# Performance work log

Measured on AMD Instinct MI355X. Metric: run time of the kernel, lower is better.

The kernel has to match this reference:

```python
import jax, jax.numpy as jnp
import numpy as np

M = 64            # multiplicity of 0e and 1o node irreps
NODE_DIM = M + 3 * M  # 256
NUM_BASIS = 8
CUTOFF = 5.0
HIDDEN = 64
NUM_W = 4 * M     # tp weight_numel: 4 uvu paths, M weights each
EPS = 1e-5


def setup_inputs() -> dict:
    key = jax.random.key(0)
    ks = jax.random.split(key, 16)
    N, E = 40000, 640000
    node_feats = jax.random.normal(ks[0], (N, NODE_DIM), dtype=jnp.float32)
    edge_index = jax.random.randint(ks[1], (2, E), 0, N)
    edge_vectors = jax.random.normal(ks[2], (E, 3), dtype=jnp.float32)
    edge_lengths = jax.random.uniform(ks[3], (E,), minval=0.5, maxval=CUTOFF, dtype=jnp.float32)
    # radial MLP params (num_basis -> hidden -> hidden -> NUM_W, SiLU)
    mlp_w1 = jax.random.normal(ks[4], (NUM_BASIS, HIDDEN), dtype=jnp.float32) / np.sqrt(NUM_BASIS)
    mlp_b1 = jnp.zeros((HIDDEN,), jnp.float32)
    mlp_w2 = jax.random.normal(ks[5], (HIDDEN, HIDDEN), dtype=jnp.float32) / np.sqrt(HIDDEN)
    mlp_b2 = jnp.zeros((HIDDEN,), jnp.float32)
    mlp_w3 = jax.random.normal(ks[6], (HIDDEN, NUM_W), dtype=jnp.float32) / np.sqrt(HIDDEN)
    mlp_b3 = jnp.zeros((NUM_W,), jnp.float32)
    # equivariant linear: per-irrep channel mixing
    lin_w0 = jax.random.normal(ks[7], (M, M), dtype=jnp.float32)
    lin_w1 = jax.random.normal(ks[8], (M, M), dtype=jnp.float32)
    # equivariant layer norm affine params
    gamma0 = jnp.ones((M,), jnp.float32)
    beta0 = jnp.zeros((M,), jnp.float32)
    gamma1 = jnp.ones((M,), jnp.float32)
    return dict(node_feats=node_feats, edge_index=edge_index, edge_vectors=edge_vectors,
                edge_lengths=edge_lengths, mlp_w1=mlp_w1, mlp_b1=mlp_b1, mlp_w2=mlp_w2,
                mlp_b2=mlp_b2, mlp_w3=mlp_w3, mlp_b3=mlp_b3, lin_w0=lin_w0, lin_w1=lin_w1,
                gamma0=gamma0, beta0=beta0, gamma1=gamma1)


def reference(node_feats, edge_index, edge_vectors, edge_lengths,
              mlp_w1, mlp_b1, mlp_w2, mlp_b2, mlp_w3, mlp_b3,
              lin_w0, lin_w1, gamma0, beta0, gamma1):
    N = node_feats.shape[0]
    row, col = edge_index[0], edge_index[1]

    # spherical harmonics of normalized edge vectors, 'component' normalization
    unit = edge_vectors / jnp.linalg.norm(edge_vectors, axis=-1, keepdims=True)
    sh1 = jnp.sqrt(3.0) * unit                                     # [E,3]; sh0 == 1

    # Bessel radial basis on edge lengths
    n = jnp.arange(1, NUM_BASIS + 1, dtype=node_feats.dtype)
    r = edge_lengths[:, None]
    rbf = jnp.sqrt(2.0 / CUTOFF) * jnp.sin(n * jnp.pi * r / CUTOFF) / r  # [E,B]

    # polynomial envelope (DimeNet, p=5)
    u = edge_lengths / CUTOFF
    env = jnp.where(u < 1.0, 1.0 - 21.0 * u**5 + 35.0 * u**6 - 15.0 * u**7, 0.0)[:, None]

    # radial MLP -> per-edge tensor-product weights, enveloped
    h = jax.nn.silu(rbf @ mlp_w1 + mlp_b1)
    h = jax.nn.silu(h @ mlp_w2 + mlp_b2)
    tp_w = (h @ mlp_w3 + mlp_b3) * env                             # [E, 4M]
    wa, wb, wc, wd = jnp.split(tp_w, 4, axis=-1)                   # each [E,M]

    # gather sender features
    s0 = node_feats[row, :M]                                       # [E,M]   0e block
    s1 = node_feats[row, M:].reshape(-1, M, 3)                     # [E,M,3] 1o block

    # weighted uvu tensor product, path-normalized (2 paths per output irrep)
    inv_s2 = 1.0 / jnp.sqrt(2.0)
    m0 = (wa * s0 + wd * jnp.einsum('emi,ei->em', s1, sh1)) * inv_s2        # [E,M]
    m1 = (wb[:, :, None] * s1 + wc[:, :, None] * s0[:, :, None] * sh1[:, None, :]) * inv_s2
    messages = jnp.concatenate([m0, m1.reshape(-1, 3 * M)], axis=-1)        # [E,256]

    # scatter-add to receivers
    agg = jax.ops.segment_sum(messages, col, num_segments=N)       # [N,256]

    # equivariant linear: mix multiplicities per irrep, fan-in normalized
    a0 = (agg[:, :M] @ lin_w0) / jnp.sqrt(jnp.asarray(M, node_feats.dtype))
    a1 = jnp.einsum('nmi,mk->nki', agg[:, M:].reshape(N, M, 3), lin_w1) \
         / jnp.sqrt(jnp.asarray(M, node_feats.dtype))

    # equivariant layer norm: standard LN on scalars, RMS-of-norms on vectors
    mu = a0.mean(axis=-1, keepdims=True)
    var = ((a0 - mu) ** 2).mean(axis=-1, keepdims=True)
    o0 = gamma0 * (a0 - mu) / jnp.sqrt(var + EPS) + beta0
    vnorm2 = (a1 ** 2).sum(-1)                                     # [N,M]
    rms = jnp.sqrt(vnorm2.mean(-1, keepdims=True) + EPS)           # [N,1]
    o1 = gamma1[None, :, None] * a1 / rms[:, :, None]

    out = jnp.concatenate([o0, o1.reshape(N, 3 * M)], axis=-1)
    return node_feats + out
```

## Files before the change

kernel.cpp:

```cpp
#include <hip/hip_runtime.h>
#include <hip/hip_fp16.h>

#define NDIM 256
#define LUT_N 2048
#define LUT_BLOCKS (LUT_N / 4)
#define SCAN_BLK 1024

typedef _Float16 h2 __attribute__((ext_vector_type(2)));
union HU { unsigned u; h2 h; };

__device__ __forceinline__ float fdot2f(unsigned a_bits, unsigned b_bits, float c)
{
    HU a, b; a.u = a_bits; b.u = b_bits;
#if __has_builtin(__builtin_amdgcn_fdot2)
    return __builtin_amdgcn_fdot2(a.h, b.h, c, false);
#else
    return fmaf((float)a.h.x, (float)b.h.x, fmaf((float)a.h.y, (float)b.h.y, c));
#endif
}

__global__ __launch_bounds__(256) void prep_kernel(
    const float* __restrict__ w1, const float* __restrict__ b1,
    const float* __restrict__ w2, const float* __restrict__ b2,
    const float* __restrict__ w3, const float* __restrict__ b3,
    uint4* __restrict__ lutp,
    const int* __restrict__ col, int E,
    int* __restrict__ counts, int* __restrict__ rank,
    const float* __restrict__ nf, uint2* __restrict__ nft,
    int histBlocks, int N)
{
    if (blockIdx.x >= (unsigned)(LUT_BLOCKS + histBlocks)) {
        int t = (blockIdx.x - LUT_BLOCKS - histBlocks) * 256 + threadIdx.x;
        if (t < N * 64) {
            int n = t >> 6, m = t & 63;
            const float* nr = nf + (size_t)n * NDIM;
            float s0 = nr[m];
            float3 s1 = ((const float3*)(nr + 64))[m];
            HU a, b;
            a.h = h2{(_Float16)s1.x, (_Float16)s1.y};
            b.h = h2{(_Float16)s1.z, (_Float16)s0};
            nft[t] = make_uint2(a.u, b.u);
        }
        return;
    }
    if (blockIdx.x >= (unsigned)LUT_BLOCKS) {
        int i = (blockIdx.x - LUT_BLOCKS) * 256 + threadIdx.x;
        if (i < E) rank[i] = atomicAdd(&counts[col[i]], 1);
        return;
    }

    __shared__ float h1[4][2][64];
    __shared__ float hh2[4][2][64];
    int tid = threadIdx.x;
    int wave = tid >> 6;
    int j = tid & 63;
    int p = blockIdx.x * 4 + wave;
    int pn = (p < LUT_N - 1) ? p + 1 : p;
    const float step = 4.5f / (float)(LUT_N - 1);
    float ra = 0.5f + step * (float)p;
    float rb = 0.5f + step * (float)pn;

    const float cnorm = 0.6324555320336759f;
    float acca = b1[j], accb = acca;
    #pragma unroll
    for (int k = 0; k < 8; ++k) {
        float freq = (float)(k + 1) * (3.14159265358979323846f / 5.0f);
        float wv = w1[k * 64 + j];
        acca = fmaf(cnorm * sinf(freq * ra) / ra, wv, acca);
        accb = fmaf(cnorm * sinf(freq * rb) / rb, wv, accb);
    }
    h1[wave][0][j] = acca / (1.0f + expf(-acca));
    h1[wave][1][j] = accb / (1.0f + expf(-accb));
    __syncthreads();

    acca = b2[j]; accb = acca;
    #pragma unroll 8
    for (int m = 0; m < 64; ++m) {
        float wv = w2[m * 64 + j];
        acca = fmaf(h1[wave][0][m], wv, acca);
        accb = fmaf(h1[wave][1][m], wv, accb);
    }
    hh2[wave][0][j] = acca / (1.0f + expf(-acca));
    hh2[wave][1][j] = accb / (1.0f + expf(-accb));
    __syncthreads();

    float ua = ra * 0.2f, ub = rb * 0.2f;
    float ua5 = ua * ua * ua * ua * ua, ub5 = ub * ub * ub * ub * ub;
    float enva = (ua < 1.0f) ? (1.0f - 21.0f * ua5 + 35.0f * ua5 * ua - 15.0f * ua5 * ua * ua) : 0.0f;
    float envb = (ub < 1.0f) ? (1.0f - 21.0f * ub5 + 35.0f * ub5 * ub - 15.0f * ub5 * ub * ub) : 0.0f;

    uint4 o;
    unsigned* ow = &o.x;
    #pragma unroll
    for (int q = 0; q < 4; ++q) {
        float oa = b3[q * 64 + j], ob = oa;
        #pragma unroll 8
        for (int m = 0; m < 64; ++m) {
            float wv = w3[m * 256 + q * 64 + j];
            oa = fmaf(hh2[wave][0][m], wv, oa);
            ob = fmaf(hh2[wave][1][m], wv, ob);
        }
        oa *= enva; ob *= envb;
        HU u; u.h = h2{(_Float16)oa, (_Float16)(ob - oa)};
        ow[q] = u.u;
    }
    lutp[p * 64 + j] = o;
}

__global__ __launch_bounds__(SCAN_BLK) void scan1_kernel(
    const int* __restrict__ counts, int* __restrict__ loc,
    int* __restrict__ btot, int N)
{
    __shared__ int sh[SCAN_BLK];
    int t = threadIdx.x;
    int idx = blockIdx.x * SCAN_BLK + t;
    int v = (idx < N) ? counts[idx] : 0;
    sh[t] = v;
    __syncthreads();
    int acc = v;
    for (int o = 1; o < SCAN_BLK; o <<= 1) {
        int add = (t >= o) ? sh[t - o] : 0;
        __syncthreads();
        acc += add;
        sh[t] = acc;
        __syncthreads();
    }
    if (idx <= N) loc[idx] = acc - v;
    if (t == SCAN_BLK - 1) btot[blockIdx.x] = acc;
}

__global__ __launch_bounds__(64) void scan2_kernel(
    const int* __restrict__ btot, int* __restrict__ off, int nb)
{
    int t = threadIdx.x;
    int v = (t < nb) ? btot[t] : 0;
    int acc = v;
    #pragma unroll
    for (int o = 1; o < 64; o <<= 1) {
        int up = __shfl_up(acc, o);
        if (t >= o) acc += up;
    }
    if (t <= nb) off[t] = acc - v;
}

__global__ void scatter_kernel(const int* __restrict__ row, const int* __restrict__ col,
                               const float* __restrict__ evec, const float* __restrict__ elen,
                               int E, const int* __restrict__ loc, const int* __restrict__ off,
                               const int* __restrict__ rank, uint4* __restrict__ em)
{
    int i = blockIdx.x * 256 + threadIdx.x;
    if (i < E) {
        int c = col[i];
        int p = loc[c] + off[c >> 10] + rank[i];
        float vx = evec[3 * i + 0], vy = evec[3 * i + 1], vz = evec[3 * i + 2];
        float inv = rsqrtf(vx * vx + vy * vy + vz * vz) * 1.7320508075688772f;
        float x = (elen[i] - 0.5f) * ((float)(LUT_N - 1) / 4.5f);
        x = fminf(fmaxf(x, 0.0f), (float)(LUT_N - 1) - 1.0e-3f);
        int i0 = (int)x;
        if (i0 > LUT_N - 2) i0 = LUT_N - 2;
        float fr = x - (float)i0;
        HU a, b;
        a.h = h2{(_Float16)(vx * inv), (_Float16)(vy * inv)};
        b.h = h2{(_Float16)(vz * inv), (_Float16)fr};
        unsigned packed = (unsigned)row[i] | ((unsigned)i0 << 16);
        em[p] = make_uint4(a.u, b.u, packed, 0u);
    }
}

struct St {
    uint4 L;
    uint2 sv;
    unsigned sh_xy, sh_zf;
};

__device__ __forceinline__ St stage_load(int j, int lane,
                                         const uint4* __restrict__ em,
                                         const uint4* __restrict__ lutp,
                                         const uint2* __restrict__ nft)
{
    St s;
    uint4 md = em[j];
    s.sh_xy = md.x;
    s.sh_zf = md.y;
    int rsrc = (int)(md.z & 0xFFFFu);
    int i0 = (int)(md.z >> 16);
    s.L = lutp[i0 * 64 + lane];
    s.sv = nft[(size_t)rsrc * 64 + lane];
    return s;
}

__device__ __forceinline__ void accum_st(const St& s, float& acc0, float& accx,
                                         float& accy, float& accz)
{
    unsigned one_f = (s.sh_zf & 0xFFFF0000u) | 0x3C00u;
    unsigned shz_0 = (s.sh_zf & 0x0000FFFFu);

    float wa = fdot2f(s.L.x, one_f, 0.0f);
    float wb = fdot2f(s.L.y, one_f, 0.0f);
    float wc = fdot2f(s.L.z, one_f, 0.0f);
    float wd = fdot2f(s.L.w, one_f, 0.0f);

    float dot = fdot2f(s.sv.x, s.sh_xy, 0.0f);
    dot = fdot2f(s.sv.y, shz_0, dot);

    HU svxy, svzs, shxy, shzf;
    svxy.u = s.sv.x; svzs.u = s.sv.y; shxy.u = s.sh_xy; shzf.u = s.sh_zf;
    float s0 = (float)svzs.h.y;

    acc0 = fmaf(wa, s0, fmaf(wd, dot, acc0));
    float wcs0 = wc * s0;
    accx = fmaf(wb, (float)svxy.h.x, fmaf(wcs0, (float)shxy.h.x, accx));
    accy = fmaf(wb, (float)svxy.h.y, fmaf(wcs0, (float)shxy.h.y, accy));
    accz = fmaf(wb, (float)svzs.h.x, fmaf(wcs0, (float)shzf.h.x, accz));
}

__global__ __launch_bounds__(256) void node_kernel(
    const float* __restrict__ nf,
    const uint2* __restrict__ nft,
    const uint4* __restrict__ lutp,
    const int* __restrict__ loc,
    const int* __restrict__ off,
    const uint4* __restrict__ em,
    const float* __restrict__ lw0,
    const float* __restrict__ lw1,
    const float* __restrict__ g0,
    const float* __restrict__ be0,
    const float* __restrict__ g1,
    float* __restrict__ out,
    int N)
{
    __shared__ float4 s_agg[4][64];
    int tid = threadIdx.x;
    int wave = tid >> 6;
    int lane = tid & 63;
    int n = blockIdx.x * 4 + wave;
    if (n >= N) return;
    float4* ag = s_agg[wave];

    int start = loc[n] + off[n >> 10];
    int end   = loc[n + 1] + off[(n + 1) >> 10];

    float acc0 = 0.0f, accx = 0.0f, accy = 0.0f, accz = 0.0f;

    int j = start;
    if (end - start >= 4) {
        St s0 = stage_load(j + 0, lane, em, lutp, nft);
        St s1 = stage_load(j + 1, lane, em, lutp, nft);
        St s2 = stage_load(j + 2, lane, em, lutp, nft);
        St s3 = stage_load(j + 3, lane, em, lutp, nft);
        for (; j + 8 <= end; j += 4) {
            accum_st(s0, acc0, accx, accy, accz); s0 = stage_load(j + 4, lane, em, lutp, nft);
            accum_st(s1, acc0, accx, accy, accz); s1 = stage_load(j + 5, lane, em, lutp, nft);
            accum_st(s2, acc0, accx, accy, accz); s2 = stage_load(j + 6, lane, em, lutp, nft);
            accum_st(s3, acc0, accx, accy, accz); s3 = stage_load(j + 7, lane, em, lutp, nft);
        }
        accum_st(s0, acc0, accx, accy, accz);
        accum_st(s1, acc0, accx, accy, accz);
        accum_st(s2, acc0, accx, accy, accz);
        accum_st(s3, acc0, accx, accy, accz);
        j += 4;
    }
    for (; j < end; ++j) {
        St s = stage_load(j, lane, em, lutp, nft);
        accum_st(s, acc0, accx, accy, accz);
    }

    const float INVS2 = 0.7071067811865476f;
    ag[lane] = make_float4(acc0 * INVS2, accx * INVS2, accy * INVS2, accz * INVS2);

    float a0 = 0.0f, t1x = 0.0f, t1y = 0.0f, t1z = 0.0f;
    #pragma unroll 8
    for (int m = 0; m < 64; ++m) {
        float w0v = lw0[m * 64 + lane];
        float w1v = lw1[m * 64 + lane];
        float4 g = ag[m];
        a0  = fmaf(g.x, w0v, a0);
        t1x = fmaf(g.y, w1v, t1x);
        t1y = fmaf(g.z, w1v, t1y);
        t1z = fmaf(g.w, w1v, t1z);
    }
    const float sc = 0.125f;
    a0 *= sc; t1x *= sc; t1y *= sc; t1z *= sc;

    float mu = a0;
    #pragma unroll
    for (int o = 32; o > 0; o >>= 1) mu += __shfl_xor(mu, o);
    mu *= (1.0f / 64.0f);
    float d = a0 - mu;
    float var = d * d;
    #pragma unroll
    for (int o = 32; o > 0; o >>= 1) var += __shfl_xor(var, o);
    var *= (1.0f / 64.0f);
    float o0 = g0[lane] * d * rsqrtf(var + 1e-5f) + be0[lane];

    float vn = t1x * t1x + t1y * t1y + t1z * t1z;
    float ms = vn;
    #pragma unroll
    for (int o = 32; o > 0; o >>= 1) ms += __shfl_xor(ms, o);
    ms *= (1.0f / 64.0f);
    float rinv = rsqrtf(ms + 1e-5f);
    float gg = g1[lane];

    size_t b = (size_t)n * NDIM;
    out[b + lane] = nf[b + lane] + o0;
    float3 rv = ((const float3*)(nf + b + 64))[lane];
    float3 ov;
    ov.x = rv.x + gg * t1x * rinv;
    ov.y = rv.y + gg * t1y * rinv;
    ov.z = rv.z + gg * t1z * rinv;
    ((float3*)(out + b + 64))[lane] = ov;
}

extern "C" void kernel_launch(void* const* d_in, const int* in_sizes, int n_in,
                              void* d_out, int out_size, void* d_ws, size_t ws_size,
                              hipStream_t stream)
{
    const float* nf   = (const float*)d_in[0];
    const int*   eidx = (const int*)d_in[1];
    const float* evec = (const float*)d_in[2];
    const float* elen = (const float*)d_in[3];
    const float* w1   = (const float*)d_in[4];
    const float* b1   = (const float*)d_in[5];
    const float* w2   = (const float*)d_in[6];
    const float* b2   = (const float*)d_in[7];
    const float* w3   = (const float*)d_in[8];
    const float* b3   = (const float*)d_in[9];
    const float* lw0  = (const float*)d_in[10];
    const float* lw1  = (const float*)d_in[11];
    const float* g0   = (const float*)d_in[12];
    const float* be0  = (const float*)d_in[13];
    const float* g1   = (const float*)d_in[14];

    int N = in_sizes[0] / NDIM;
    int E = in_sizes[3];

    int nb = (N + SCAN_BLK) / SCAN_BLK;

    char* ws = (char*)d_ws;
    size_t off_b = 0;
    auto align256 = [&]() { off_b = (off_b + 255) & ~(size_t)255; };
    uint4* lutp = (uint4*)(ws + off_b);   off_b += (size_t)LUT_N * 64 * 16;   align256();
    int* counts = (int*)(ws + off_b);     off_b += (size_t)N * 4;             align256();
    int* loc = (int*)(ws + off_b);        off_b += (size_t)(N + 1) * 4;       align256();
    int* btot = (int*)(ws + off_b);       off_b += (size_t)nb * 4;            align256();
    int* boff = (int*)(ws + off_b);       off_b += (size_t)(nb + 1) * 4;      align256();
    int* rank = (int*)(ws + off_b);       off_b += (size_t)E * 4;             align256();
    uint4* em = (uint4*)(ws + off_b);     off_b += (size_t)E * 16;            align256();
    uint2* nft = (uint2*)(ws + off_b);    off_b += (size_t)N * 64 * 8;

    const int* row = eidx;
    const int* col = eidx + E;

    int histBlocks = (E + 255) / 256;
    int tBlocks = (N * 64 + 255) / 256;

    hipMemsetAsync(counts, 0, (size_t)N * 4, stream);
    prep_kernel<<<LUT_BLOCKS + histBlocks + tBlocks, 256, 0, stream>>>(
        w1, b1, w2, b2, w3, b3, lutp, col, E, counts, rank, nf, nft, histBlocks, N);
    scan1_kernel<<<nb, SCAN_BLK, 0, stream>>>(counts, loc, btot, N);
    scan2_kernel<<<1, 64, 0, stream>>>(btot, boff, nb);
    scatter_kernel<<<(E + 255) / 256, 256, 0, stream>>>(row, col, evec, elen, E,
                                                        loc, boff, rank, em);
    node_kernel<<<(N + 3) / 4, 256, 0, stream>>>(nf, nft, lutp, loc, boff, em,
                                                 lw0, lw1, g0, be0, g1,
                                                 (float*)d_out, N);
}
```

Before: 178.8 us.

## Fold block-offset scan into consumers, precompute fp16 weights, deepen edge prefetch

Removes the separate scan2 launch: each wave in the scatter and node kernels now redoes the small block-total prefix scan with shuffles and picks its offset with __shfl. The scatter stage also stores a ready-made (1, frac) fp16 pair in the spare word of each edge record, which saves bit manipulation in the inner accumulate. The node kernel's software prefetch grows from 4 to 8 in-flight edges, and the segment bounds are made wave-uniform with readfirstlane. The cost is redundant scan work in every wave and higher register pressure from the deeper prefetch.

```diff
diff --git a/kernel.cpp b/kernel.cpp
--- a/kernel.cpp
+++ b/kernel.cpp
@@ -129,29 +129,31 @@
     if (t == SCAN_BLK - 1) btot[blockIdx.x] = acc;
 }
 
-__global__ __launch_bounds__(64) void scan2_kernel(
-    const int* __restrict__ btot, int* __restrict__ off, int nb)
-{
-    int t = threadIdx.x;
-    int v = (t < nb) ? btot[t] : 0;
+__device__ __forceinline__ int btot_scan(const int* __restrict__ btot, int nb, int lane)
+{
+    int v = (lane < nb) ? btot[lane] : 0;
     int acc = v;
     #pragma unroll
     for (int o = 1; o < 64; o <<= 1) {
         int up = __shfl_up(acc, o);
-        if (t >= o) acc += up;
-    }
-    if (t <= nb) off[t] = acc - v;
-}
-
-__global__ void scatter_kernel(const int* __restrict__ row, const int* __restrict__ col,
-                               const float* __restrict__ evec, const float* __restrict__ elen,
-                               int E, const int* __restrict__ loc, const int* __restrict__ off,
-                               const int* __restrict__ rank, uint4* __restrict__ em)
-{
+        if (lane >= o) acc += up;
+    }
+    return acc - v;
+}
+
+__global__ __launch_bounds__(256) void scatter_kernel(
+    const int* __restrict__ row, const int* __restrict__ col,
+    const float* __restrict__ evec, const float* __restrict__ elen,
+    int E, const int* __restrict__ loc, const int* __restrict__ btot, int nb,
+    const int* __restrict__ rank, uint4* __restrict__ em)
+{
+    int lane = threadIdx.x & 63;
+    int excl = btot_scan(btot, nb, lane);
+
     int i = blockIdx.x * 256 + threadIdx.x;
     if (i < E) {
         int c = col[i];
-        int p = loc[c] + off[c >> 10] + rank[i];
+        int p = loc[c] + __shfl(excl, c >> 10) + rank[i];
         float vx = evec[3 * i + 0], vy = evec[3 * i + 1], vz = evec[3 * i + 2];
         float inv = rsqrtf(vx * vx + vy * vy + vz * vz) * 1.7320508075688772f;
         float x = (elen[i] - 0.5f) * ((float)(LUT_N - 1) / 4.5f);
@@ -159,18 +161,19 @@
         int i0 = (int)x;
         if (i0 > LUT_N - 2) i0 = LUT_N - 2;
         float fr = x - (float)i0;
-        HU a, b;
+        HU a, b, w;
         a.h = h2{(_Float16)(vx * inv), (_Float16)(vy * inv)};
-        b.h = h2{(_Float16)(vz * inv), (_Float16)fr};
+        b.h = h2{(_Float16)(vz * inv), (_Float16)0.0f};
+        w.h = h2{(_Float16)1.0f, (_Float16)fr};
         unsigned packed = (unsigned)row[i] | ((unsigned)i0 << 16);
-        em[p] = make_uint4(a.u, b.u, packed, 0u);
+        em[p] = make_uint4(a.u, b.u, packed, w.u);
     }
 }
 
 struct St {
     uint4 L;
     uint2 sv;
-    unsigned sh_xy, sh_zf;
+    unsigned sh_xy, sh_z0, one_f;
 };
 
 __device__ __forceinline__ St stage_load(int j, int lane,
@@ -181,7 +184,8 @@
     St s;
     uint4 md = em[j];
     s.sh_xy = md.x;
-    s.sh_zf = md.y;
+    s.sh_z0 = md.y;
+    s.one_f = md.w;
     int rsrc = (int)(md.z & 0xFFFFu);
     int i0 = (int)(md.z >> 16);
     s.L = lutp[i0 * 64 + lane];
@@ -192,26 +196,23 @@
 __device__ __forceinline__ void accum_st(const St& s, float& acc0, float& accx,
                                          float& accy, float& accz)
 {
-    unsigned one_f = (s.sh_zf & 0xFFFF0000u) | 0x3C00u;
-    unsigned shz_0 = (s.sh_zf & 0x0000FFFFu);
-
-    float wa = fdot2f(s.L.x, one_f, 0.0f);
-    float wb = fdot2f(s.L.y, one_f, 0.0f);
-    float wc = fdot2f(s.L.z, one_f, 0.0f);
-    float wd = fdot2f(s.L.w, one_f, 0.0f);
+    float wa = fdot2f(s.L.x, s.one_f, 0.0f);
+    float wb = fdot2f(s.L.y, s.one_f, 0.0f);
+    float wc = fdot2f(s.L.z, s.one_f, 0.0f);
+    float wd = fdot2f(s.L.w, s.one_f, 0.0f);
 
     float dot = fdot2f(s.sv.x, s.sh_xy, 0.0f);
-    dot = fdot2f(s.sv.y, shz_0, dot);
-
-    HU svxy, svzs, shxy, shzf;
-    svxy.u = s.sv.x; svzs.u = s.sv.y; shxy.u = s.sh_xy; shzf.u = s.sh_zf;
+    dot = fdot2f(s.sv.y, s.sh_z0, dot);
+
+    HU svxy, svzs, shxy, shz0;
+    svxy.u = s.sv.x; svzs.u = s.sv.y; shxy.u = s.sh_xy; shz0.u = s.sh_z0;
     float s0 = (float)svzs.h.y;
 
     acc0 = fmaf(wa, s0, fmaf(wd, dot, acc0));
     float wcs0 = wc * s0;
     accx = fmaf(wb, (float)svxy.h.x, fmaf(wcs0, (float)shxy.h.x, accx));
     accy = fmaf(wb, (float)svxy.h.y, fmaf(wcs0, (float)shxy.h.y, accy));
-    accz = fmaf(wb, (float)svzs.h.x, fmaf(wcs0, (float)shzf.h.x, accz));
+    accz = fmaf(wb, (float)svzs.h.x, fmaf(wcs0, (float)shz0.h.x, accz));
 }
 
 __global__ __launch_bounds__(256) void node_kernel(
@@ -219,7 +220,7 @@
     const uint2* __restrict__ nft,
     const uint4* __restrict__ lutp,
     const int* __restrict__ loc,
-    const int* __restrict__ off,
+    const int* __restrict__ btot, int nb,
     const uint4* __restrict__ em,
     const float* __restrict__ lw0,
     const float* __restrict__ lw1,
@@ -234,31 +235,48 @@
     int wave = tid >> 6;
     int lane = tid & 63;
     int n = blockIdx.x * 4 + wave;
+
+    int excl = btot_scan(btot, nb, lane);
+
     if (n >= N) return;
     float4* ag = s_agg[wave];
 
-    int start = loc[n] + off[n >> 10];
-    int end   = loc[n + 1] + off[(n + 1) >> 10];
+    int start = loc[n]     + __shfl(excl, n >> 10);
+    int end   = loc[n + 1] + __shfl(excl, (n + 1) >> 10);
+    start = __builtin_amdgcn_readfirstlane(start);
+    end   = __builtin_amdgcn_readfirstlane(end);
 
     float acc0 = 0.0f, accx = 0.0f, accy = 0.0f, accz = 0.0f;
 
     int j = start;
-    if (end - start >= 4) {
+    if (end - start >= 8) {
         St s0 = stage_load(j + 0, lane, em, lutp, nft);
         St s1 = stage_load(j + 1, lane, em, lutp, nft);
         St s2 = stage_load(j + 2, lane, em, lutp, nft);
         St s3 = stage_load(j + 3, lane, em, lutp, nft);
-        for (; j + 8 <= end; j += 4) {
-            accum_st(s0, acc0, accx, accy, accz); s0 = stage_load(j + 4, lane, em, lutp, nft);
-            accum_st(s1, acc0, accx, accy, accz); s1 = stage_load(j + 5, lane, em, lutp, nft);
-            accum_st(s2, acc0, accx, accy, accz); s2 = stage_load(j + 6, lane, em, lutp, nft);
-            accum_st(s3, acc0, accx, accy, accz); s3 = stage_load(j + 7, lane, em, lutp, nft);
+        St s4 = stage_load(j + 4, lane, em, lutp, nft);
+        St s5 = stage_load(j + 5, lane, em, lutp, nft);
+        St s6 = stage_load(j + 6, lane, em, lutp, nft);
+        St s7 = stage_load(j + 7, lane, em, lutp, nft);
+        for (; j + 16 <= end; j += 8) {
+            accum_st(s0, acc0, accx, accy, accz); s0 = stage_load(j +  8, lane, em, lutp, nft);
+            accum_st(s1, acc0, accx, accy, accz); s1 = stage_load(j +  9, lane, em, lutp, nft);
+            accum_st(s2, acc0, accx, accy, accz); s2 = stage_load(j + 10, lane, em, lutp, nft);
+            accum_st(s3, acc0, accx, accy, accz); s3 = stage_load(j + 11, lane, em, lutp, nft);
+            accum_st(s4, acc0, accx, accy, accz); s4 = stage_load(j + 12, lane, em, lutp, nft);
+            accum_st(s5, acc0, accx, accy, accz); s5 = stage_load(j + 13, lane, em, lutp, nft);
+            accum_st(s6, acc0, accx, accy, accz); s6 = stage_load(j + 14, lane, em, lutp, nft);
+            accum_st(s7, acc0, accx, accy, accz); s7 = stage_load(j + 15, lane, em, lutp, nft);
         }
         accum_st(s0, acc0, accx, accy, accz);
         accum_st(s1, acc0, accx, accy, accz);
         accum_st(s2, acc0, accx, accy, accz);
         accum_st(s3, acc0, accx, accy, accz);
-        j += 4;
+        accum_st(s4, acc0, accx, accy, accz);
+        accum_st(s5, acc0, accx, accy, accz);
+        accum_st(s6, acc0, accx, accy, accz);
+        accum_st(s7, acc0, accx, accy, accz);
+        j += 8;
     }
     for (; j < end; ++j) {
         St s = stage_load(j, lane, em, lutp, nft);
@@ -343,7 +361,6 @@
     int* counts = (int*)(ws + off_b);     off_b += (size_t)N * 4;             align256();
     int* loc = (int*)(ws + off_b);        off_b += (size_t)(N + 1) * 4;       align256();
     int* btot = (int*)(ws + off_b);       off_b += (size_t)nb * 4;            align256();
-    int* boff = (int*)(ws + off_b);       off_b += (size_t)(nb + 1) * 4;      align256();
     int* rank = (int*)(ws + off_b);       off_b += (size_t)E * 4;             align256();
     uint4* em = (uint4*)(ws + off_b);     off_b += (size_t)E * 16;            align256();
     uint2* nft = (uint2*)(ws + off_b);    off_b += (size_t)N * 64 * 8;
@@ -358,10 +375,9 @@
     prep_kernel<<<LUT_BLOCKS + histBlocks + tBlocks, 256, 0, stream>>>(
         w1, b1, w2, b2, w3, b3, lutp, col, E, counts, rank, nf, nft, histBlocks, N);
     scan1_kernel<<<nb, SCAN_BLK, 0, stream>>>(counts, loc, btot, N);
-    scan2_kernel<<<1, 64, 0, stream>>>(btot, boff, nb);
     scatter_kernel<<<(E + 255) / 256, 256, 0, stream>>>(row, col, evec, elen, E,
-                                                        loc, boff, rank, em);
-    node_kernel<<<(N + 3) / 4, 256, 0, stream>>>(nf, nft, lutp, loc, boff, em,
+                                                        loc, btot, nb, rank, em);
+    node_kernel<<<(N + 3) / 4, 256, 0, stream>>>(nf, nft, lutp, loc, btot, nb, em,
                                                  lw0, lw1, g0, be0, g1,
                                                  (float*)d_out, N);
 }
```

Result: faster. 169.5 us (-5.2%).
